# Performance work log

Measured on AMD Instinct MI355X. Metric: run time of the kernel, lower is better.

The kernel has to match this reference:

```python
import jax, jax.numpy as jnp
import numpy as np

N, E, F, H, C = 100000, 1600000, 128, 16, 40


def setup_inputs() -> dict:
    key = jax.random.key(0)
    ks = jax.random.split(key, 10)
    x = jax.random.normal(ks[0], (N, F), dtype=jnp.float32)
    edge_index = jax.random.randint(ks[1], (2, E), 0, N, dtype=jnp.int64)
    edge_weight = jax.random.uniform(ks[2], (E,), dtype=jnp.float32)
    s = 0.1
    return {
        "x": x,
        "edge_index": edge_index,
        "edge_weight": edge_weight,  # unused by SAGEConv, kept for signature fidelity
        "W_l1": jax.random.normal(ks[3], (F, H), dtype=jnp.float32) * s,
        "b1": jax.random.normal(ks[4], (H,), dtype=jnp.float32) * s,
        "W_r1": jax.random.normal(ks[5], (F, H), dtype=jnp.float32) * s,
        "W_l2": jax.random.normal(ks[6], (H, C), dtype=jnp.float32) * s,
        "b2": jax.random.normal(ks[7], (C,), dtype=jnp.float32) * s,
        "W_r2": jax.random.normal(ks[8], (H, C), dtype=jnp.float32) * s,
    }


def _sage_conv(x, src, dst, W_l, b, W_r):
    # PyG SAGEConv (aggr='mean', root_weight=True):
    #   out = lin_l(mean_{j in N(i)} x_j) + lin_r(x_i)
    n = x.shape[0]
    msg = x[src]                                              # [E, d] gather
    s = jax.ops.segment_sum(msg, dst, num_segments=n)         # [N, d]
    cnt = jax.ops.segment_sum(jnp.ones((src.shape[0],), x.dtype), dst,
                              num_segments=n)                 # [N]
    agg = s / jnp.maximum(cnt, 1.0)[:, None]                  # mean aggregation
    return agg @ W_l + b + x @ W_r


def reference(x, edge_index, edge_weight, W_l1, b1, W_r1, W_l2, b2, W_r2):
    src, dst = edge_index[0], edge_index[1]
    h = jax.nn.relu(_sage_conv(x, src, dst, W_l1, b1, W_r1))
    # F.dropout(training=self.training) is identity in eval mode
    out = _sage_conv(h, src, dst, W_l2, b2, W_r2)
    return jax.nn.log_softmax(out, axis=1)
```

## Files before the change

### kernel.cpp

```cpp
#include <hip/hip_runtime.h>
#include <hip/hip_fp16.h>
#include <math.h>

namespace {
constexpr int kN = 100000;
constexpr int kE = 1600000;
constexpr int kF = 128;
constexpr int kH = 16;
constexpr int kC = 40;
constexpr int kCap = 48;

constexpr int kBins = 392;
constexpr int kSplitBlocks = 200;
constexpr int kBE = 8000;
constexpr int kChunkCap = 56;

__global__ __launch_bounds__(512) void split_kernel(
    const int* __restrict__ src,
    const int* __restrict__ dst,
    unsigned* __restrict__ binbuf,
    int* __restrict__ cnt2)
{
    __shared__ int hist[kBins];
    __shared__ int cur2[kBins];
    __shared__ int pfx[kBins];
    __shared__ int sc[512];
    __shared__ unsigned stage[kBE];

    int tid = threadIdx.x, blk = blockIdx.x;
    if (tid < kBins) hist[tid] = 0;
    __syncthreads();

    unsigned pr[16];
    int pb[16];
    int e0 = blk * kBE;
#pragma unroll
    for (int k = 0; k < 16; ++k) {
        int local = k * 512 + tid;
        if (local < kBE) {
            int e = e0 + local;
            int s = src[e];
            int d = dst[e];
            pr[k] = ((unsigned)s << 8) | (unsigned)(d & 255);
            pb[k] = d >> 8;
            atomicAdd(&hist[pb[k]], 1);
        } else {
            pb[k] = -1;
        }
    }
    __syncthreads();

    int v = (tid < kBins) ? hist[tid] : 0;
    sc[tid] = v;
    __syncthreads();
    for (int off = 1; off < 512; off <<= 1) {
        int t = (tid >= off) ? sc[tid - off] : 0;
        __syncthreads();
        sc[tid] += t;
        __syncthreads();
    }
    if (tid < kBins) {
        int ex = sc[tid] - v;
        pfx[tid] = ex;
        cur2[tid] = ex;
    }
    __syncthreads();

#pragma unroll
    for (int k = 0; k < 16; ++k) {
        if (pb[k] >= 0) {
            int pos = atomicAdd(&cur2[pb[k]], 1);
            stage[pos] = pr[k];
        }
    }
    __syncthreads();

    for (int j = tid; j < kBE; j += 512) {
        unsigned u = stage[j];
        int lo = 0, hi = kBins - 1;
        while (lo < hi) {
            int mid = (lo + hi + 1) >> 1;
            if (pfx[mid] <= j) lo = mid; else hi = mid - 1;
        }
        int b = lo;
        int ofs = j - pfx[b];
        if (ofs < kChunkCap)
            binbuf[(size_t)(b * kSplitBlocks + blk) * kChunkCap + ofs] = u;
    }
    if (tid < kBins) {
        int c = hist[tid];
        cnt2[tid * kSplitBlocks + blk] = c > kChunkCap ? kChunkCap : c;
    }
}

__global__ __launch_bounds__(512) void build_proj_kernel(
    const unsigned* __restrict__ binbuf,
    const int* __restrict__ cnt2,
    int* __restrict__ eidx,
    int* __restrict__ cnt,
    const float* __restrict__ x,
    const float* __restrict__ Wl,
    const float* __restrict__ Wr,
    __half* __restrict__ p1,
    __half* __restrict__ r1)
{
    __shared__ float sW[2 * kF * kH];
    __shared__ int cur[256];

    int tid = threadIdx.x;
    int b = blockIdx.x;

    if ((b & 1) == 0) {
        int bin = b >> 1;
        if (tid < 256) cur[tid] = 0;
        __syncthreads();
        int wave = tid >> 6, lane = tid & 63;
        int base_node = bin << 8;
        for (int ci = wave; ci < kSplitBlocks; ci += 8) {
            int cbase = bin * kSplitBlocks + ci;
            int c = cnt2[cbase];
            if (lane < c) {
                unsigned u = binbuf[(size_t)cbase * kChunkCap + lane];
                int dl = (int)(u & 255u);
                int s  = (int)(u >> 8);
                int p = atomicAdd(&cur[dl], 1);
                if (p < kCap) eidx[(size_t)(base_node + dl) * kCap + p] = s;
            }
        }
        __syncthreads();
        if (tid < 256) {
            int node = base_node + tid;
            if (node < kN) cnt[node] = cur[tid];
        }
        return;
    }

    int pb = b >> 1;
    if (pb >= 196) return;
    for (int i = tid; i < kF * kH; i += 512) {
        sW[i] = Wl[i];
        sW[kF * kH + i] = Wr[i];
    }
    __syncthreads();
    int node = pb * 512 + tid;
    if (node >= kN) return;
    const float4* xr = reinterpret_cast<const float4*>(x + (size_t)node * kF);
    float accL[kH];
    float accR[kH];
#pragma unroll
    for (int j = 0; j < kH; ++j) { accL[j] = 0.f; accR[j] = 0.f; }
    for (int k4 = 0; k4 < kF / 4; ++k4) {
        float4 vx = xr[k4];
        float vv[4] = {vx.x, vx.y, vx.z, vx.w};
#pragma unroll
        for (int u = 0; u < 4; ++u) {
            const float* wl = &sW[(k4 * 4 + u) * kH];
            const float* wr = &sW[kF * kH + (k4 * 4 + u) * kH];
            float s = vv[u];
#pragma unroll
            for (int j = 0; j < kH; ++j) {
                accL[j] = fmaf(s, wl[j], accL[j]);
                accR[j] = fmaf(s, wr[j], accR[j]);
            }
        }
    }
    union { __half2 h2[8]; float4 f4[2]; } uL, uR;
#pragma unroll
    for (int q = 0; q < 8; ++q) {
        uL.h2[q] = __floats2half2_rn(accL[2*q], accL[2*q+1]);
        uR.h2[q] = __floats2half2_rn(accR[2*q], accR[2*q+1]);
    }
    float4* p1r = reinterpret_cast<float4*>(p1 + (size_t)node * kH);
    p1r[0] = uL.f4[0];
    p1r[1] = uL.f4[1];
    float4* r1r = reinterpret_cast<float4*>(r1 + (size_t)node * kH);
    r1r[0] = uR.f4[0];
    r1r[1] = uR.f4[1];
}

union Sl { float2 f2; __half2 h2[2]; };

__global__ __launch_bounds__(256) void gather1_kernel(
    const int* __restrict__ cnt,
    const int* __restrict__ eidx,
    const __half* __restrict__ p1,
    const __half* __restrict__ r1,
    const float* __restrict__ b1,
    __half* __restrict__ h)
{
    int t = blockIdx.x * 256 + threadIdx.x;
    int node = t >> 2, part = t & 3;
    if (node >= kN) return;
    int dgr = cnt[node];
    int m = dgr > kCap ? kCap : dgr;
    const int* ep = eidx + (size_t)node * kCap;

    float a0 = 0.f, a1 = 0.f, a2 = 0.f, a3 = 0.f;
    int i = 0;
    for (; i + 4 <= m; i += 4) {
        int4 e4 = *reinterpret_cast<const int4*>(ep + i);
        Sl w0, w1, w2, w3;
        w0.f2 = *reinterpret_cast<const float2*>(p1 + (size_t)e4.x * kH + part * 4);
        w1.f2 = *reinterpret_cast<const float2*>(p1 + (size_t)e4.y * kH + part * 4);
        w2.f2 = *reinterpret_cast<const float2*>(p1 + (size_t)e4.z * kH + part * 4);
        w3.f2 = *reinterpret_cast<const float2*>(p1 + (size_t)e4.w * kH + part * 4);
        float2 u0 = __half22float2(w0.h2[0]), v0 = __half22float2(w0.h2[1]);
        float2 u1 = __half22float2(w1.h2[0]), v1 = __half22float2(w1.h2[1]);
        float2 u2 = __half22float2(w2.h2[0]), v2 = __half22float2(w2.h2[1]);
        float2 u3 = __half22float2(w3.h2[0]), v3 = __half22float2(w3.h2[1]);
        a0 += (u0.x + u1.x) + (u2.x + u3.x);
        a1 += (u0.y + u1.y) + (u2.y + u3.y);
        a2 += (v0.x + v1.x) + (v2.x + v3.x);
        a3 += (v0.y + v1.y) + (v2.y + v3.y);
    }
    for (; i < m; ++i) {
        Sl w;
        w.f2 = *reinterpret_cast<const float2*>(p1 + (size_t)ep[i] * kH + part * 4);
        float2 u = __half22float2(w.h2[0]), v = __half22float2(w.h2[1]);
        a0 += u.x; a1 += u.y; a2 += v.x; a3 += v.y;
    }

    float inv = 1.0f / fmaxf((float)dgr, 1.0f);
    Sl rs;
    rs.f2 = *reinterpret_cast<const float2*>(r1 + (size_t)node * kH + part * 4);
    float2 ru = __half22float2(rs.h2[0]), rv = __half22float2(rs.h2[1]);
    float4 bv = reinterpret_cast<const float4*>(b1)[part];
    float o0 = fmaxf(fmaf(a0, inv, bv.x + ru.x), 0.f);
    float o1 = fmaxf(fmaf(a1, inv, bv.y + ru.y), 0.f);
    float o2 = fmaxf(fmaf(a2, inv, bv.z + rv.x), 0.f);
    float o3 = fmaxf(fmaf(a3, inv, bv.w + rv.y), 0.f);
    Sl ws;
    ws.h2[0] = __floats2half2_rn(o0, o1);
    ws.h2[1] = __floats2half2_rn(o2, o3);
    *reinterpret_cast<float2*>(h + (size_t)node * kH + part * 4) = ws.f2;
}

__global__ __launch_bounds__(256) void gather2_out_kernel(
    const int* __restrict__ cnt,
    const int* __restrict__ eidx,
    const __half* __restrict__ h,
    const float* __restrict__ Wl,
    const float* __restrict__ b2,
    const float* __restrict__ Wr,
    float* __restrict__ out)
{
    __shared__ float sWl[kH * kC];
    __shared__ float sWr[kH * kC];
    __shared__ float sb[kC];
    __shared__ float sA[64][17];
    __shared__ float sH[64][17];
    for (int i = threadIdx.x; i < kH * kC; i += 256) {
        sWl[i] = Wl[i];
        sWr[i] = Wr[i];
    }
    if (threadIdx.x < kC) sb[threadIdx.x] = b2[threadIdx.x];

    int t = blockIdx.x * 256 + threadIdx.x;
    int node = t >> 2, part = t & 3, g = threadIdx.x >> 2;
    bool active = node < kN;

    if (active) {
        int dgr = cnt[node];
        int m = dgr > kCap ? kCap : dgr;
        const int* ep = eidx + (size_t)node * kCap;
        float a0 = 0.f, a1 = 0.f, a2 = 0.f, a3 = 0.f;
        int i = 0;
        for (; i + 4 <= m; i += 4) {
            int4 e4 = *reinterpret_cast<const int4*>(ep + i);
            Sl w0, w1, w2, w3;
            w0.f2 = *reinterpret_cast<const float2*>(h + (size_t)e4.x * kH + part * 4);
            w1.f2 = *reinterpret_cast<const float2*>(h + (size_t)e4.y * kH + part * 4);
            w2.f2 = *reinterpret_cast<const float2*>(h + (size_t)e4.z * kH + part * 4);
            w3.f2 = *reinterpret_cast<const float2*>(h + (size_t)e4.w * kH + part * 4);
            float2 u0 = __half22float2(w0.h2[0]), v0 = __half22float2(w0.h2[1]);
            float2 u1 = __half22float2(w1.h2[0]), v1 = __half22float2(w1.h2[1]);
            float2 u2 = __half22float2(w2.h2[0]), v2 = __half22float2(w2.h2[1]);
            float2 u3 = __half22float2(w3.h2[0]), v3 = __half22float2(w3.h2[1]);
            a0 += (u0.x + u1.x) + (u2.x + u3.x);
            a1 += (u0.y + u1.y) + (u2.y + u3.y);
            a2 += (v0.x + v1.x) + (v2.x + v3.x);
            a3 += (v0.y + v1.y) + (v2.y + v3.y);
        }
        for (; i < m; ++i) {
            Sl w;
            w.f2 = *reinterpret_cast<const float2*>(h + (size_t)ep[i] * kH + part * 4);
            float2 u = __half22float2(w.h2[0]), v = __half22float2(w.h2[1]);
            a0 += u.x; a1 += u.y; a2 += v.x; a3 += v.y;
        }
        float inv = 1.0f / fmaxf((float)dgr, 1.0f);
        Sl hs;
        hs.f2 = *reinterpret_cast<const float2*>(h + (size_t)node * kH + part * 4);
        float2 hu = __half22float2(hs.h2[0]), hv = __half22float2(hs.h2[1]);
        int f0 = part * 4;
        sA[g][f0 + 0] = a0 * inv;
        sA[g][f0 + 1] = a1 * inv;
        sA[g][f0 + 2] = a2 * inv;
        sA[g][f0 + 3] = a3 * inv;
        sH[g][f0 + 0] = hu.x;
        sH[g][f0 + 1] = hu.y;
        sH[g][f0 + 2] = hv.x;
        sH[g][f0 + 3] = hv.y;
    }
    __syncthreads();
    if (!active) return;

    int j0 = part * 10;
    float o[10];
#pragma unroll
    for (int jj = 0; jj < 10; ++jj) o[jj] = sb[j0 + jj];
    for (int k = 0; k < kH; ++k) {
        float av = sA[g][k];
        float hv = sH[g][k];
        const float* wl = &sWl[k * kC + j0];
        const float* wr = &sWr[k * kC + j0];
#pragma unroll
        for (int jj = 0; jj < 10; ++jj)
            o[jj] += av * wl[jj] + hv * wr[jj];
    }
    float mx = o[0];
#pragma unroll
    for (int jj = 1; jj < 10; ++jj) mx = fmaxf(mx, o[jj]);
    mx = fmaxf(mx, __shfl_xor(mx, 1));
    mx = fmaxf(mx, __shfl_xor(mx, 2));
    float ssum = 0.f;
#pragma unroll
    for (int jj = 0; jj < 10; ++jj) ssum += expf(o[jj] - mx);
    ssum += __shfl_xor(ssum, 1);
    ssum += __shfl_xor(ssum, 2);
    float ls = mx + logf(ssum);
    float2* op = reinterpret_cast<float2*>(out + (size_t)node * kC + j0);
#pragma unroll
    for (int q = 0; q < 5; ++q)
        op[q] = make_float2(o[2*q] - ls, o[2*q+1] - ls);
}

}

extern "C" void kernel_launch(void* const* d_in, const int* in_sizes, int n_in,
                              void* d_out, int out_size, void* d_ws, size_t ws_size,
                              hipStream_t stream)
{
    const float* x   = (const float*)d_in[0];
    const int*   ei  = (const int*)d_in[1];
    const float* Wl1 = (const float*)d_in[3];
    const float* b1  = (const float*)d_in[4];
    const float* Wr1 = (const float*)d_in[5];
    const float* Wl2 = (const float*)d_in[6];
    const float* b2  = (const float*)d_in[7];
    const float* Wr2 = (const float*)d_in[8];
    float* out = (float*)d_out;

    char* ws = (char*)d_ws;
    size_t off = 0;
    auto alloc = [&](size_t bytes) -> void* {
        char* p = ws + off;
        off += (bytes + 255) & ~(size_t)255;
        return (void*)p;
    };
    int*      cnt    = (int*)alloc((size_t)kN * sizeof(int));
    int*      eidx   = (int*)alloc((size_t)kN * kCap * sizeof(int));
    __half*   p1h    = (__half*)alloc((size_t)kN * kH * sizeof(__half));
    __half*   r1h    = (__half*)alloc((size_t)kN * kH * sizeof(__half));
    unsigned* binbuf = (unsigned*)alloc((size_t)kBins * kSplitBlocks * kChunkCap * 4);
    int*      cnt2   = (int*)alloc((size_t)kBins * kSplitBlocks * sizeof(int));
    __half*   hh     = (__half*)binbuf;

    const int* srcp = ei;
    const int* dstp = ei + kE;

    split_kernel<<<kSplitBlocks, 512, 0, stream>>>(srcp, dstp, binbuf, cnt2);
    build_proj_kernel<<<2 * kBins, 512, 0, stream>>>(
        binbuf, cnt2, eidx, cnt, x, Wl1, Wr1, p1h, r1h);
    gather1_kernel<<<(kN * 4 + 255) / 256, 256, 0, stream>>>(cnt, eidx, p1h, r1h, b1, hh);
    gather2_out_kernel<<<(kN * 4 + 255) / 256, 256, 0, stream>>>(cnt, eidx, hh, Wl2, b2, Wr2, out);
}
```

Measured before the change: 235.1 us.

## Fuse CSR build with layer-1 gather via shared-memory adjacency lists

The x@W projection now runs in its own kernel ahead of the edge split. The bucket-build kernel keeps each bin's adjacency lists in shared memory and performs the layer-1 mean aggregation directly from them, so the separate gather1 launch and its reread of eidx go away. The split kernel also records a coarse bin id per staged edge, which replaces the binary search over prefix sums. In exchange, build_g1 needs about 50KB of LDS per block, which lowers occupancy, and the gather loop is unrolled less, which weakens latency hiding. h also gets its own buffer instead of aliasing binbuf.

```diff
diff --git a/kernel.cpp b/kernel.cpp
--- a/kernel.cpp
+++ b/kernel.cpp
@@ -15,6 +15,54 @@
 constexpr int kBE = 8000;
 constexpr int kChunkCap = 56;
 
+__global__ __launch_bounds__(256) void proj_kernel(
+    const float* __restrict__ x,
+    const float* __restrict__ Wl,
+    const float* __restrict__ Wr,
+    __half* __restrict__ p1,
+    __half* __restrict__ r1)
+{
+    __shared__ float sW[2 * kF * kH];
+    for (int i = threadIdx.x; i < kF * kH; i += 256) {
+        sW[i] = Wl[i];
+        sW[kF * kH + i] = Wr[i];
+    }
+    __syncthreads();
+    int node = blockIdx.x * 256 + threadIdx.x;
+    if (node >= kN) return;
+    const float4* xr = reinterpret_cast<const float4*>(x + (size_t)node * kF);
+    float accL[kH], accR[kH];
+#pragma unroll
+    for (int j = 0; j < kH; ++j) { accL[j] = 0.f; accR[j] = 0.f; }
+    for (int k4 = 0; k4 < kF / 4; ++k4) {
+        float4 vx = xr[k4];
+        float vv[4] = {vx.x, vx.y, vx.z, vx.w};
+#pragma unroll
+        for (int u = 0; u < 4; ++u) {
+            const float* wl = &sW[(k4 * 4 + u) * kH];
+            const float* wr = &sW[kF * kH + (k4 * 4 + u) * kH];
+            float s = vv[u];
+#pragma unroll
+            for (int j = 0; j < kH; ++j) {
+                accL[j] = fmaf(s, wl[j], accL[j]);
+                accR[j] = fmaf(s, wr[j], accR[j]);
+            }
+        }
+    }
+    union { __half2 h2[8]; float4 f4[2]; } uL, uR;
+#pragma unroll
+    for (int q = 0; q < 8; ++q) {
+        uL.h2[q] = __floats2half2_rn(accL[2*q], accL[2*q+1]);
+        uR.h2[q] = __floats2half2_rn(accR[2*q], accR[2*q+1]);
+    }
+    float4* p1r = reinterpret_cast<float4*>(p1 + (size_t)node * kH);
+    p1r[0] = uL.f4[0];
+    p1r[1] = uL.f4[1];
+    float4* r1r = reinterpret_cast<float4*>(r1 + (size_t)node * kH);
+    r1r[0] = uR.f4[0];
+    r1r[1] = uR.f4[1];
+}
+
 __global__ __launch_bounds__(512) void split_kernel(
     const int* __restrict__ src,
     const int* __restrict__ dst,
@@ -26,6 +74,7 @@
     __shared__ int pfx[kBins];
     __shared__ int sc[512];
     __shared__ unsigned stage[kBE];
+    __shared__ unsigned char binid[kBE];
 
     int tid = threadIdx.x, blk = blockIdx.x;
     if (tid < kBins) hist[tid] = 0;
@@ -71,18 +120,15 @@
         if (pb[k] >= 0) {
             int pos = atomicAdd(&cur2[pb[k]], 1);
             stage[pos] = pr[k];
+            binid[pos] = (unsigned char)(pb[k] >> 1);
         }
     }
     __syncthreads();
 
     for (int j = tid; j < kBE; j += 512) {
         unsigned u = stage[j];
-        int lo = 0, hi = kBins - 1;
-        while (lo < hi) {
-            int mid = (lo + hi + 1) >> 1;
-            if (pfx[mid] <= j) lo = mid; else hi = mid - 1;
-        }
-        int b = lo;
+        int b = (int)binid[j] * 2;
+        if (b + 1 < kBins && pfx[b + 1] <= j) b += 1;
         int ofs = j - pfx[b];
         if (ofs < kChunkCap)
             binbuf[(size_t)(b * kSplitBlocks + blk) * kChunkCap + ofs] = u;
@@ -93,147 +139,86 @@
     }
 }
 
-__global__ __launch_bounds__(512) void build_proj_kernel(
+__global__ __launch_bounds__(512) void build_g1_kernel(
     const unsigned* __restrict__ binbuf,
     const int* __restrict__ cnt2,
     int* __restrict__ eidx,
     int* __restrict__ cnt,
-    const float* __restrict__ x,
-    const float* __restrict__ Wl,
-    const float* __restrict__ Wr,
-    __half* __restrict__ p1,
-    __half* __restrict__ r1)
-{
-    __shared__ float sW[2 * kF * kH];
-    __shared__ int cur[256];
-
-    int tid = threadIdx.x;
-    int b = blockIdx.x;
-
-    if ((b & 1) == 0) {
-        int bin = b >> 1;
-        if (tid < 256) cur[tid] = 0;
-        __syncthreads();
-        int wave = tid >> 6, lane = tid & 63;
-        int base_node = bin << 8;
-        for (int ci = wave; ci < kSplitBlocks; ci += 8) {
-            int cbase = bin * kSplitBlocks + ci;
-            int c = cnt2[cbase];
-            if (lane < c) {
-                unsigned u = binbuf[(size_t)cbase * kChunkCap + lane];
-                int dl = (int)(u & 255u);
-                int s  = (int)(u >> 8);
-                int p = atomicAdd(&cur[dl], 1);
-                if (p < kCap) eidx[(size_t)(base_node + dl) * kCap + p] = s;
-            }
-        }
-        __syncthreads();
-        if (tid < 256) {
-            int node = base_node + tid;
-            if (node < kN) cnt[node] = cur[tid];
-        }
-        return;
-    }
-
-    int pb = b >> 1;
-    if (pb >= 196) return;
-    for (int i = tid; i < kF * kH; i += 512) {
-        sW[i] = Wl[i];
-        sW[kF * kH + i] = Wr[i];
-    }
-    __syncthreads();
-    int node = pb * 512 + tid;
-    if (node >= kN) return;
-    const float4* xr = reinterpret_cast<const float4*>(x + (size_t)node * kF);
-    float accL[kH];
-    float accR[kH];
-#pragma unroll
-    for (int j = 0; j < kH; ++j) { accL[j] = 0.f; accR[j] = 0.f; }
-    for (int k4 = 0; k4 < kF / 4; ++k4) {
-        float4 vx = xr[k4];
-        float vv[4] = {vx.x, vx.y, vx.z, vx.w};
-#pragma unroll
-        for (int u = 0; u < 4; ++u) {
-            const float* wl = &sW[(k4 * 4 + u) * kH];
-            const float* wr = &sW[kF * kH + (k4 * 4 + u) * kH];
-            float s = vv[u];
-#pragma unroll
-            for (int j = 0; j < kH; ++j) {
-                accL[j] = fmaf(s, wl[j], accL[j]);
-                accR[j] = fmaf(s, wr[j], accR[j]);
-            }
-        }
-    }
-    union { __half2 h2[8]; float4 f4[2]; } uL, uR;
-#pragma unroll
-    for (int q = 0; q < 8; ++q) {
-        uL.h2[q] = __floats2half2_rn(accL[2*q], accL[2*q+1]);
-        uR.h2[q] = __floats2half2_rn(accR[2*q], accR[2*q+1]);
-    }
-    float4* p1r = reinterpret_cast<float4*>(p1 + (size_t)node * kH);
-    p1r[0] = uL.f4[0];
-    p1r[1] = uL.f4[1];
-    float4* r1r = reinterpret_cast<float4*>(r1 + (size_t)node * kH);
-    r1r[0] = uR.f4[0];
-    r1r[1] = uR.f4[1];
-}
-
-union Sl { float2 f2; __half2 h2[2]; };
-
-__global__ __launch_bounds__(256) void gather1_kernel(
-    const int* __restrict__ cnt,
-    const int* __restrict__ eidx,
     const __half* __restrict__ p1,
     const __half* __restrict__ r1,
     const float* __restrict__ b1,
     __half* __restrict__ h)
 {
-    int t = blockIdx.x * 256 + threadIdx.x;
-    int node = t >> 2, part = t & 3;
-    if (node >= kN) return;
-    int dgr = cnt[node];
-    int m = dgr > kCap ? kCap : dgr;
-    const int* ep = eidx + (size_t)node * kCap;
-
-    float a0 = 0.f, a1 = 0.f, a2 = 0.f, a3 = 0.f;
-    int i = 0;
-    for (; i + 4 <= m; i += 4) {
-        int4 e4 = *reinterpret_cast<const int4*>(ep + i);
-        Sl w0, w1, w2, w3;
-        w0.f2 = *reinterpret_cast<const float2*>(p1 + (size_t)e4.x * kH + part * 4);
-        w1.f2 = *reinterpret_cast<const float2*>(p1 + (size_t)e4.y * kH + part * 4);
-        w2.f2 = *reinterpret_cast<const float2*>(p1 + (size_t)e4.z * kH + part * 4);
-        w3.f2 = *reinterpret_cast<const float2*>(p1 + (size_t)e4.w * kH + part * 4);
-        float2 u0 = __half22float2(w0.h2[0]), v0 = __half22float2(w0.h2[1]);
-        float2 u1 = __half22float2(w1.h2[0]), v1 = __half22float2(w1.h2[1]);
-        float2 u2 = __half22float2(w2.h2[0]), v2 = __half22float2(w2.h2[1]);
-        float2 u3 = __half22float2(w3.h2[0]), v3 = __half22float2(w3.h2[1]);
-        a0 += (u0.x + u1.x) + (u2.x + u3.x);
-        a1 += (u0.y + u1.y) + (u2.y + u3.y);
-        a2 += (v0.x + v1.x) + (v2.x + v3.x);
-        a3 += (v0.y + v1.y) + (v2.y + v3.y);
-    }
-    for (; i < m; ++i) {
-        Sl w;
-        w.f2 = *reinterpret_cast<const float2*>(p1 + (size_t)ep[i] * kH + part * 4);
-        float2 u = __half22float2(w.h2[0]), v = __half22float2(w.h2[1]);
-        a0 += u.x; a1 += u.y; a2 += v.x; a3 += v.y;
-    }
-
-    float inv = 1.0f / fmaxf((float)dgr, 1.0f);
-    Sl rs;
-    rs.f2 = *reinterpret_cast<const float2*>(r1 + (size_t)node * kH + part * 4);
-    float2 ru = __half22float2(rs.h2[0]), rv = __half22float2(rs.h2[1]);
-    float4 bv = reinterpret_cast<const float4*>(b1)[part];
-    float o0 = fmaxf(fmaf(a0, inv, bv.x + ru.x), 0.f);
-    float o1 = fmaxf(fmaf(a1, inv, bv.y + ru.y), 0.f);
-    float o2 = fmaxf(fmaf(a2, inv, bv.z + rv.x), 0.f);
-    float o3 = fmaxf(fmaf(a3, inv, bv.w + rv.y), 0.f);
-    Sl ws;
-    ws.h2[0] = __floats2half2_rn(o0, o1);
-    ws.h2[1] = __floats2half2_rn(o2, o3);
-    *reinterpret_cast<float2*>(h + (size_t)node * kH + part * 4) = ws.f2;
-}
+    __shared__ int lists[256][kCap];
+    __shared__ int cur[256];
+    __shared__ int scnt2[kSplitBlocks];
+
+    int tid = threadIdx.x;
+    int bin = blockIdx.x;
+    int base_node = bin << 8;
+
+    if (tid < 256) cur[tid] = 0;
+    if (tid < kSplitBlocks) scnt2[tid] = cnt2[bin * kSplitBlocks + tid];
+    else if (tid >= 512 - (kSplitBlocks - (512 - 256)) && false) {}
+    __syncthreads();
+
+    int wave = tid >> 6, lane = tid & 63;
+    for (int ci = wave; ci < kSplitBlocks; ci += 8) {
+        int c = scnt2[ci];
+        if (lane < c) {
+            unsigned u = binbuf[(size_t)(bin * kSplitBlocks + ci) * kChunkCap + lane];
+            int dl = (int)(u & 255u);
+            int s  = (int)(u >> 8);
+            int p = atomicAdd(&cur[dl], 1);
+            if (p < kCap) lists[dl][p] = s;
+        }
+    }
+    __syncthreads();
+
+    if (tid < 256) {
+        int node = base_node + tid;
+        if (node < kN) cnt[node] = cur[tid];
+    }
+    for (int j = tid; j < 256 * kCap; j += 512) {
+        int dl = j / kCap, slot = j % kCap;
+        int m = cur[dl] < kCap ? cur[dl] : kCap;
+        int node = base_node + dl;
+        if (slot < m && node < kN)
+            eidx[(size_t)node * kCap + slot] = lists[dl][slot];
+    }
+
+    for (int r = 0; r < 2; ++r) {
+        int unit = r * 512 + tid;
+        int dl = unit >> 2, part = unit & 3;
+        int node = base_node + dl;
+        if (node >= kN) continue;
+        int dgr = cur[dl];
+        int m = dgr > kCap ? kCap : dgr;
+        float a0 = 0.f, a1 = 0.f, a2 = 0.f, a3 = 0.f;
+        for (int i = 0; i < m; ++i) {
+            int s = lists[dl][i];
+            union { float2 f2; __half2 h2[2]; } w;
+            w.f2 = *reinterpret_cast<const float2*>(p1 + (size_t)s * kH + part * 4);
+            float2 u = __half22float2(w.h2[0]), vv = __half22float2(w.h2[1]);
+            a0 += u.x; a1 += u.y; a2 += vv.x; a3 += vv.y;
+        }
+        float inv = 1.0f / fmaxf((float)dgr, 1.0f);
+        union { float2 f2; __half2 h2[2]; } rs;
+        rs.f2 = *reinterpret_cast<const float2*>(r1 + (size_t)node * kH + part * 4);
+        float2 ru = __half22float2(rs.h2[0]), rv = __half22float2(rs.h2[1]);
+        float4 bv = reinterpret_cast<const float4*>(b1)[part];
+        float o0 = fmaxf(fmaf(a0, inv, bv.x + ru.x), 0.f);
+        float o1 = fmaxf(fmaf(a1, inv, bv.y + ru.y), 0.f);
+        float o2 = fmaxf(fmaf(a2, inv, bv.z + rv.x), 0.f);
+        float o3 = fmaxf(fmaf(a3, inv, bv.w + rv.y), 0.f);
+        union { float2 f2; __half2 h2[2]; } ws;
+        ws.h2[0] = __floats2half2_rn(o0, o1);
+        ws.h2[1] = __floats2half2_rn(o2, o3);
+        *reinterpret_cast<float2*>(h + (size_t)node * kH + part * 4) = ws.f2;
+    }
+}
+
+union Sl { float2 f2; __half2 h2[2]; };
 
 __global__ __launch_bounds__(256) void gather2_out_kernel(
     const int* __restrict__ cnt,
@@ -361,16 +346,15 @@
     int*      eidx   = (int*)alloc((size_t)kN * kCap * sizeof(int));
     __half*   p1h    = (__half*)alloc((size_t)kN * kH * sizeof(__half));
     __half*   r1h    = (__half*)alloc((size_t)kN * kH * sizeof(__half));
+    __half*   hh     = (__half*)alloc((size_t)kN * kH * sizeof(__half));
     unsigned* binbuf = (unsigned*)alloc((size_t)kBins * kSplitBlocks * kChunkCap * 4);
     int*      cnt2   = (int*)alloc((size_t)kBins * kSplitBlocks * sizeof(int));
-    __half*   hh     = (__half*)binbuf;
 
     const int* srcp = ei;
     const int* dstp = ei + kE;
 
+    proj_kernel<<<(kN + 255) / 256, 256, 0, stream>>>(x, Wl1, Wr1, p1h, r1h);
     split_kernel<<<kSplitBlocks, 512, 0, stream>>>(srcp, dstp, binbuf, cnt2);
-    build_proj_kernel<<<2 * kBins, 512, 0, stream>>>(
-        binbuf, cnt2, eidx, cnt, x, Wl1, Wr1, p1h, r1h);
-    gather1_kernel<<<(kN * 4 + 255) / 256, 256, 0, stream>>>(cnt, eidx, p1h, r1h, b1, hh);
+    build_g1_kernel<<<kBins, 512, 0, stream>>>(binbuf, cnt2, eidx, cnt, p1h, r1h, b1, hh);
     gather2_out_kernel<<<(kN * 4 + 255) / 256, 256, 0, stream>>>(cnt, eidx, hh, Wl2, b2, Wr2, out);
 }
```

Result: faster. 210.3 us (-10.5%).
